# Performance work log

Hardware: AMD Instinct MI355X
Metric: run time of the kernel (lower is better)

## Reference

```python
import jax, jax.numpy as jnp
import numpy as np

N = 100000


def gcn_conv(x, edge_index, W, b):
    """PyG GCNConv: add self-loops, symmetric normalization, x @ W, aggregate, + bias."""
    n = x.shape[0]
    src = jnp.concatenate([edge_index[0], jnp.arange(n)])
    dst = jnp.concatenate([edge_index[1], jnp.arange(n)])
    deg = jax.ops.segment_sum(jnp.ones_like(dst, dtype=x.dtype), dst, num_segments=n)
    dinv = jnp.where(deg > 0, jax.lax.rsqrt(deg), 0.0)
    norm = dinv[src] * dinv[dst]  # [E+N]
    h = x @ W  # [N, out]
    msg = h[src] * norm[:, None]  # gather + scale
    agg = jax.ops.segment_sum(msg, dst, num_segments=n)
    return agg + b


def setup_inputs() -> dict:
    key = jax.random.key(0)
    ks = jax.random.split(key, 10)
    x = jax.random.normal(ks[0], (N, 256), dtype=jnp.float32)
    edge_index = jax.random.randint(ks[1], (2, 3200000), 0, N, dtype=jnp.int64)
    def glorot(k, fan_in, fan_out):
        s = np.sqrt(6.0 / (fan_in + fan_out)).astype(np.float32)
        return jax.random.uniform(k, (fan_in, fan_out), jnp.float32, -s, s)
    return {
        "x": x,
        "edge_index": edge_index,
        "W1": glorot(ks[2], 256, 128), "b1": jnp.zeros((128,), jnp.float32),
        "W2": glorot(ks[3], 128, 64), "b2": jnp.zeros((64,), jnp.float32),
        "W3": glorot(ks[4], 64, 16), "b3": jnp.zeros((16,), jnp.float32),
        "Wc": glorot(ks[5], 16, 2), "bc": jnp.zeros((2,), jnp.float32),
    }


def reference(x, edge_index, W1, b1, W2, b2, W3, b3, Wc, bc):
    h = jnp.tanh(gcn_conv(x, edge_index, W1, b1))
    h = jnp.tanh(gcn_conv(h, edge_index, W2, b2))
    h = jnp.tanh(gcn_conv(h, edge_index, W3, b3))
    out = h @ Wc + bc
    return (out, h)
```

## Files before the change

### kernel.cpp

```cpp
#include <hip/hip_runtime.h>
#include <hip/hip_fp16.h>
#include <cstdint>
#include <cstddef>


#define EPB 16384
#define BSHIFT 8
#define NBUC_MAX 512
#define BCAP 12800

typedef __attribute__((ext_vector_type(8))) short short8;
typedef __attribute__((ext_vector_type(4))) float f32x4;

__global__ __launch_bounds__(256) void scan_block(const int* __restrict__ src, int n,
                                                  int* __restrict__ incl,
                                                  int* __restrict__ bsum) {
    int tid = threadIdx.x;
    int v = blockIdx.x * 256 + tid;
    int val = (v < n) ? src[v] : 0;
    int lane = tid & 63, w = tid >> 6;
#pragma unroll
    for (int off = 1; off < 64; off <<= 1) {
        int t = __shfl_up(val, off, 64);
        if (lane >= off) val += t;
    }
    __shared__ int wsum[4];
    if (lane == 63) wsum[w] = val;
    __syncthreads();
#pragma unroll
    for (int i = 0; i < 4; ++i)
        if (i < w) val += wsum[i];
    if (v < n) incl[v] = val;
    if (tid == 255) bsum[blockIdx.x] = val;
}

__global__ __launch_bounds__(512) void scan_sums(int* __restrict__ bsum, int nb) {
    int tid = threadIdx.x;
    int val = (tid < nb) ? bsum[tid] : 0;
    int lane = tid & 63, w = tid >> 6;
#pragma unroll
    for (int off = 1; off < 64; off <<= 1) {
        int t = __shfl_up(val, off, 64);
        if (lane >= off) val += t;
    }
    __shared__ int wsum[8];
    if (lane == 63) wsum[w] = val;
    __syncthreads();
#pragma unroll
    for (int i = 0; i < 8; ++i)
        if (i < w) val += wsum[i];
    if (tid < nb) bsum[tid] = val;
}

__global__ __launch_bounds__(256) void finalize_scan(
    const int* __restrict__ incl, const int* __restrict__ bsum,
    const int* __restrict__ src, int n, int* __restrict__ excl) {
    int v = blockIdx.x * 256 + threadIdx.x;
    if (v >= n) return;
    int boff = (blockIdx.x == 0) ? 0 : bsum[blockIdx.x - 1];
    excl[v] = boff + incl[v] - src[v];
}

__global__ __launch_bounds__(256) void hist_bucket(
    const int* __restrict__ ei, int E, int nbuc, int nch,
    int* __restrict__ histG) {
    __shared__ int h[NBUC_MAX];
    const int k = blockIdx.x;
    for (int b = threadIdx.x; b < NBUC_MAX; b += 256) h[b] = 0;
    __syncthreads();
    const int base = k * EPB, end = min(E, base + EPB);
    for (int i = base + threadIdx.x; i < end; i += 256)
        atomicAdd(&h[ei[(size_t)E + i] >> BSHIFT], 1);
    __syncthreads();
    for (int b = threadIdx.x; b < nbuc; b += 256)
        histG[(size_t)b * nch + k] = h[b];
}

__global__ __launch_bounds__(256) void bucket_scatter(
    const int* __restrict__ ei, int E, int nbuc, int nch,
    const int* __restrict__ offs, uint2* __restrict__ ebuf) {
    __shared__ int cur[NBUC_MAX];
    const int k = blockIdx.x;
    for (int b = threadIdx.x; b < nbuc; b += 256)
        cur[b] = offs[(size_t)b * nch + k];
    __syncthreads();
    const int base = k * EPB, end = min(E, base + EPB);
    for (int i = base + threadIdx.x; i < end; i += 256) {
        int s = ei[i];
        int d = ei[(size_t)E + i];
        int pos = atomicAdd(&cur[d >> BSHIFT], 1);
        ebuf[pos] = make_uint2((unsigned)s, (unsigned)d);
    }
}

__global__ __launch_bounds__(256) void bucket_build(
    const uint2* __restrict__ ebuf, const int* __restrict__ offs,
    int E, int nbuc, int nch, int n,
    int* __restrict__ col, int* __restrict__ deg,
    int* __restrict__ row_start, float* __restrict__ dinv) {
    const int b = blockIdx.x;
    const int tid = threadIdx.x;
    const int estart = offs[(size_t)b * nch];
    const int eend = (b + 1 < nbuc) ? offs[(size_t)(b + 1) * nch] : E;
    const int cnt = eend - estart;

    __shared__ int degl[256];
    __shared__ int curl[256];
    __shared__ int wsum[4];
    __shared__ int colstage[BCAP];

    degl[tid] = 0;
    __syncthreads();
    for (int i = tid; i < cnt; i += 256)
        atomicAdd(&degl[ebuf[estart + i].y & 255], 1);
    __syncthreads();
    int myDeg = degl[tid];
    int val = myDeg;
    int lane = tid & 63, w = tid >> 6;
#pragma unroll
    for (int off = 1; off < 64; off <<= 1) {
        int t = __shfl_up(val, off, 64);
        if (lane >= off) val += t;
    }
    if (lane == 63) wsum[w] = val;
    __syncthreads();
#pragma unroll
    for (int i = 0; i < 4; ++i)
        if (i < w) val += wsum[i];
    int excl = val - myDeg;
    curl[tid] = excl;
    int v = (b << BSHIFT) + tid;
    if (v < n) {
        deg[v] = myDeg;
        row_start[v] = estart + excl;
        dinv[v] = rsqrtf((float)(myDeg + 1));
    }
    __syncthreads();
    if (cnt <= BCAP) {
        for (int i = tid; i < cnt; i += 256) {
            uint2 e = ebuf[estart + i];
            int pos = atomicAdd(&curl[e.y & 255], 1);
            colstage[pos] = (int)e.x;
        }
        __syncthreads();
        for (int i = tid; i < cnt; i += 256)
            col[estart + i] = colstage[i];
    } else {
        for (int i = tid; i < cnt; i += 256) {
            uint2 e = ebuf[estart + i];
            int pos = atomicAdd(&curl[e.y & 255], 1);
            col[estart + pos] = (int)e.x;
        }
    }
}

__device__ inline unsigned int pack2h(float a, float b) {
    __half ha = __float2half_rn(a), hb = __float2half_rn(b);
    unsigned short ua = *(unsigned short*)&ha, ub = *(unsigned short*)&hb;
    return (unsigned int)ua | ((unsigned int)ub << 16);
}

__device__ inline unsigned short f32_to_bf16_rn(float f) {
    unsigned int u = __float_as_uint(f);
    unsigned int r = (u + 0x7FFFu + ((u >> 16) & 1u)) >> 16;
    return (unsigned short)r;
}
__device__ inline float bf16_to_f32(unsigned short h) {
    return __uint_as_float(((unsigned int)h) << 16);
}

template <int FIN, int FOUT>
__global__ __launch_bounds__(256) void pack_w(const float* __restrict__ W,
                                              unsigned short* __restrict__ Wpk) {
    constexpr int KC = FIN / 32, CF = FOUT / 16;
    constexpr int TOT = KC * CF * 64 * 8;
    int idx = blockIdx.x * 256 + threadIdx.x;
    if (idx >= TOT) return;
    int j = idx & 7;
    int lane = (idx >> 3) & 63;
    int cf = (idx >> 9) % CF;
    int kc = (idx >> 9) / CF;
    int k = kc * 32 + ((lane >> 4) * 8) + j;
    int c = cf * 16 + (lane & 15);
    float w = W[(size_t)k * FOUT + c];
    unsigned short h = f32_to_bf16_rn(w);
    unsigned short l = f32_to_bf16_rn(w - bf16_to_f32(h));
    size_t base = ((size_t)((kc * CF + cf) * 64 + lane)) * 16;
    Wpk[base + j] = h;
    Wpk[base + 8 + j] = l;
}

template <int FIN, int FOUT>
__global__ __launch_bounds__(256) void gemm_mfma(
    const float* __restrict__ X, const unsigned short* __restrict__ Wpk,
    const float* __restrict__ dinv, __half* __restrict__ Hs, int n) {
    constexpr int KC = FIN / 32, CF = FOUT / 16, RF = 2;
    constexpr int BM = 4 * RF * 16;
    const int w = threadIdx.x >> 6, lane = threadIdx.x & 63;
    const int g = lane >> 4, rr = lane & 15;
    const int node0 = blockIdx.x * BM + w * (RF * 16);
    const int ko = g * 8;

    f32x4 acc[RF][CF];
#pragma unroll
    for (int rf = 0; rf < RF; ++rf)
#pragma unroll
        for (int cf = 0; cf < CF; ++cf)
            acc[rf][cf] = (f32x4){0.f, 0.f, 0.f, 0.f};

    union U16 { uint4 u; short8 s; };

    for (int kc = 0; kc < KC; ++kc) {
        short8 ahi[RF], alo[RF];
#pragma unroll
        for (int rf = 0; rf < RF; ++rf) {
            int r = node0 + rf * 16 + rr;
            float xv[8] = {0.f, 0.f, 0.f, 0.f, 0.f, 0.f, 0.f, 0.f};
            if (r < n) {
                const float* xp = X + (size_t)r * FIN + kc * 32 + ko;
                float4 a0 = *(const float4*)xp;
                float4 a1 = *(const float4*)(xp + 4);
                xv[0] = a0.x; xv[1] = a0.y; xv[2] = a0.z; xv[3] = a0.w;
                xv[4] = a1.x; xv[5] = a1.y; xv[6] = a1.z; xv[7] = a1.w;
            }
#pragma unroll
            for (int j = 0; j < 8; ++j) {
                unsigned short hb = f32_to_bf16_rn(xv[j]);
                float rem = xv[j] - bf16_to_f32(hb);
                ahi[rf][j] = (short)hb;
                alo[rf][j] = (short)f32_to_bf16_rn(rem);
            }
        }
#pragma unroll
        for (int cf = 0; cf < CF; ++cf) {
            const uint4* bp = (const uint4*)(Wpk +
                ((size_t)((kc * CF + cf) * 64 + lane)) * 16);
            U16 bh, bl;
            bh.u = bp[0];
            bl.u = bp[1];
#pragma unroll
            for (int rf = 0; rf < RF; ++rf) {
                acc[rf][cf] = __builtin_amdgcn_mfma_f32_16x16x32_bf16(
                    ahi[rf], bh.s, acc[rf][cf], 0, 0, 0);
                acc[rf][cf] = __builtin_amdgcn_mfma_f32_16x16x32_bf16(
                    alo[rf], bh.s, acc[rf][cf], 0, 0, 0);
                acc[rf][cf] = __builtin_amdgcn_mfma_f32_16x16x32_bf16(
                    ahi[rf], bl.s, acc[rf][cf], 0, 0, 0);
            }
        }
    }

#pragma unroll
    for (int rf = 0; rf < RF; ++rf) {
#pragma unroll
        for (int i = 0; i < 4; ++i) {
            int r = node0 + rf * 16 + g * 4 + i;
            if (r >= n) continue;
            float di = dinv[r];
            __half* hp = Hs + (size_t)r * FOUT + rr;
#pragma unroll
            for (int cf = 0; cf < CF; ++cf)
                hp[cf * 16] = __float2half_rn(acc[rf][cf][i] * di);
        }
    }
}

template <int FIN, int FOUT, int TM>
__global__ __launch_bounds__(256) void gemm_tile_h(
    const float* __restrict__ X, const float* __restrict__ W,
    const float* __restrict__ dinv, __half* __restrict__ Hs, int n) {
    constexpr int CT = FOUT / 4;
    constexpr int RG = 256 / CT;
    static_assert(TM == RG * 4, "tile mismatch");
    constexpr int LROW = FIN + 4;
    __shared__ float xs[TM][LROW];

    const int node0 = blockIdx.x * TM;
    const int tid = threadIdx.x;

    constexpr int C4 = FIN / 4;
    for (int i = tid; i < TM * C4; i += 256) {
        int r = i / C4, c = i % C4;
        float4 v = make_float4(0.f, 0.f, 0.f, 0.f);
        if (node0 + r < n) v = *(const float4*)(X + (size_t)(node0 + r) * FIN + c * 4);
        *(float4*)&xs[r][c * 4] = v;
    }
    __syncthreads();

    const int col = (tid % CT) * 4;
    const int r0 = (tid / CT) * 4;

    float acc[4][4];
#pragma unroll
    for (int i = 0; i < 4; ++i)
#pragma unroll
        for (int j = 0; j < 4; ++j) acc[i][j] = 0.f;

#pragma unroll 2
    for (int k = 0; k < FIN; k += 4) {
        float4 w0 = *(const float4*)(W + (size_t)(k + 0) * FOUT + col);
        float4 w1 = *(const float4*)(W + (size_t)(k + 1) * FOUT + col);
        float4 w2 = *(const float4*)(W + (size_t)(k + 2) * FOUT + col);
        float4 w3 = *(const float4*)(W + (size_t)(k + 3) * FOUT + col);
        float4 av[4];
        av[0] = *(const float4*)&xs[r0 + 0][k];
        av[1] = *(const float4*)&xs[r0 + 1][k];
        av[2] = *(const float4*)&xs[r0 + 2][k];
        av[3] = *(const float4*)&xs[r0 + 3][k];
#pragma unroll
        for (int rr = 0; rr < 4; ++rr) {
            acc[rr][0] = fmaf(av[rr].x, w0.x, acc[rr][0]);
            acc[rr][1] = fmaf(av[rr].x, w0.y, acc[rr][1]);
            acc[rr][2] = fmaf(av[rr].x, w0.z, acc[rr][2]);
            acc[rr][3] = fmaf(av[rr].x, w0.w, acc[rr][3]);
            acc[rr][0] = fmaf(av[rr].y, w1.x, acc[rr][0]);
            acc[rr][1] = fmaf(av[rr].y, w1.y, acc[rr][1]);
            acc[rr][2] = fmaf(av[rr].y, w1.z, acc[rr][2]);
            acc[rr][3] = fmaf(av[rr].y, w1.w, acc[rr][3]);
            acc[rr][0] = fmaf(av[rr].z, w2.x, acc[rr][0]);
            acc[rr][1] = fmaf(av[rr].z, w2.y, acc[rr][1]);
            acc[rr][2] = fmaf(av[rr].z, w2.z, acc[rr][2]);
            acc[rr][3] = fmaf(av[rr].z, w2.w, acc[rr][3]);
            acc[rr][0] = fmaf(av[rr].w, w3.x, acc[rr][0]);
            acc[rr][1] = fmaf(av[rr].w, w3.y, acc[rr][1]);
            acc[rr][2] = fmaf(av[rr].w, w3.z, acc[rr][2]);
            acc[rr][3] = fmaf(av[rr].w, w3.w, acc[rr][3]);
        }
    }

#pragma unroll
    for (int rr = 0; rr < 4; ++rr) {
        int node = node0 + r0 + rr;
        if (node < n) {
            float di = dinv[node];
            uint2 pk;
            pk.x = pack2h(acc[rr][0] * di, acc[rr][1] * di);
            pk.y = pack2h(acc[rr][2] * di, acc[rr][3] * di);
            *(uint2*)(Hs + (size_t)node * FOUT + col) = pk;
        }
    }
}

__device__ inline void add8h(float* acc, uint4 p) {
    unsigned int w[4] = {p.x, p.y, p.z, p.w};
#pragma unroll
    for (int t = 0; t < 4; ++t) {
        __half2 h = *(const __half2*)&w[t];
        float2 f = __half22float2(h);
        acc[2 * t] += f.x;
        acc[2 * t + 1] += f.y;
    }
}

template <int F>
__global__ __launch_bounds__(256) void pull_agg_h(
    const int* __restrict__ row_start, const int* __restrict__ deg,
    const int* __restrict__ col, const __half* __restrict__ Hs,
    const float* __restrict__ dinv, const float* __restrict__ B,
    float* __restrict__ OUT, int n) {
    constexpr int TPE = F / 8;
    long long gid = (long long)blockIdx.x * 256 + threadIdx.x;
    int node = (int)(gid / TPE);
    int lane = (int)(gid % TPE);
    if (node >= n) return;
    const int beg = row_start[node];
    const int cnt = deg[node];
    const size_t lo = (size_t)lane * 8;

    float acc[8] = {0.f, 0.f, 0.f, 0.f, 0.f, 0.f, 0.f, 0.f};
    add8h(acc, *(const uint4*)(Hs + (size_t)node * F + lo));

    int j = 0;
    for (; j + 8 <= cnt; j += 8) {
        int s0 = col[beg + j + 0], s1 = col[beg + j + 1];
        int s2 = col[beg + j + 2], s3 = col[beg + j + 3];
        int s4 = col[beg + j + 4], s5 = col[beg + j + 5];
        int s6 = col[beg + j + 6], s7 = col[beg + j + 7];
        uint4 p0 = *(const uint4*)(Hs + (size_t)s0 * F + lo);
        uint4 p1 = *(const uint4*)(Hs + (size_t)s1 * F + lo);
        uint4 p2 = *(const uint4*)(Hs + (size_t)s2 * F + lo);
        uint4 p3 = *(const uint4*)(Hs + (size_t)s3 * F + lo);
        uint4 p4 = *(const uint4*)(Hs + (size_t)s4 * F + lo);
        uint4 p5 = *(const uint4*)(Hs + (size_t)s5 * F + lo);
        uint4 p6 = *(const uint4*)(Hs + (size_t)s6 * F + lo);
        uint4 p7 = *(const uint4*)(Hs + (size_t)s7 * F + lo);
        add8h(acc, p0); add8h(acc, p1); add8h(acc, p2); add8h(acc, p3);
        add8h(acc, p4); add8h(acc, p5); add8h(acc, p6); add8h(acc, p7);
    }
    for (; j < cnt; ++j) {
        int s = col[beg + j];
        add8h(acc, *(const uint4*)(Hs + (size_t)s * F + lo));
    }

    float di = dinv[node];
    float4 b0 = *(const float4*)(B + lo);
    float4 b1 = *(const float4*)(B + lo + 4);
    float4 r0, r1;
    r0.x = tanhf(fmaf(acc[0], di, b0.x));
    r0.y = tanhf(fmaf(acc[1], di, b0.y));
    r0.z = tanhf(fmaf(acc[2], di, b0.z));
    r0.w = tanhf(fmaf(acc[3], di, b0.w));
    r1.x = tanhf(fmaf(acc[4], di, b1.x));
    r1.y = tanhf(fmaf(acc[5], di, b1.y));
    r1.z = tanhf(fmaf(acc[6], di, b1.z));
    r1.w = tanhf(fmaf(acc[7], di, b1.w));
    float* op = OUT + (size_t)node * F + lo;
    *(float4*)(op) = r0;
    *(float4*)(op + 4) = r1;
}

__global__ void classifier_kernel(const float* __restrict__ Hf,
                                  const float* __restrict__ Wc,
                                  const float* __restrict__ bc,
                                  float* __restrict__ out, int n) {
    int v = blockIdx.x * blockDim.x + threadIdx.x;
    if (v >= n) return;
    float o0 = bc[0], o1 = bc[1];
    const float* h = Hf + (size_t)v * 16;
#pragma unroll
    for (int k = 0; k < 16; ++k) {
        float hv = h[k];
        o0 = fmaf(hv, Wc[k * 2 + 0], o0);
        o1 = fmaf(hv, Wc[k * 2 + 1], o1);
    }
    out[(size_t)v * 2 + 0] = o0;
    out[(size_t)v * 2 + 1] = o1;
}

extern "C" void kernel_launch(void* const* d_in, const int* in_sizes, int n_in,
                              void* d_out, int out_size, void* d_ws, size_t ws_size,
                              hipStream_t stream) {
    const float* x  = (const float*)d_in[0];
    const int* ei   = (const int*)d_in[1];
    const float* W1 = (const float*)d_in[2];
    const float* b1 = (const float*)d_in[3];
    const float* W2 = (const float*)d_in[4];
    const float* b2 = (const float*)d_in[5];
    const float* W3 = (const float*)d_in[6];
    const float* b3 = (const float*)d_in[7];
    const float* Wc = (const float*)d_in[8];
    const float* bc = (const float*)d_in[9];

    const int n = in_sizes[0] / 256;
    const int E = in_sizes[1] / 2;
    const int nbuc = (n + 255) >> BSHIFT;
    const int nch  = (E + EPB - 1) / EPB;
    const int NH   = nbuc * nch;
    const int nb2  = (NH + 255) / 256;

    float* outp = (float*)d_out;
    float* outh = outp + (size_t)n * 2;

    int*    deg       = (int*)d_ws;
    float*  dinv      = (float*)d_ws + (size_t)n;
    int*    row_start = (int*)d_ws + 2 * (size_t)n;
    int*    histG     = (int*)d_ws + 3 * (size_t)n;
    int*    incl      = histG + NH;
    int*    bsum      = incl + NH;
    int*    offs      = bsum + 512;
    int*    col       = offs + NH;
    __half* HsH       = (__half*)(col + E);
    float*  xbuf      = (float*)(HsH + (size_t)n * 128);
    uint2*  ebuf      = (uint2*)xbuf;

    unsigned short* Wpk1 = (unsigned short*)histG;
    unsigned short* Wpk2 = Wpk1 + (size_t)256 * 128 * 2;

    hist_bucket<<<nch, 256, 0, stream>>>(ei, E, nbuc, nch, histG);
    scan_block<<<nb2, 256, 0, stream>>>(histG, NH, incl, bsum);
    scan_sums<<<1, 512, 0, stream>>>(bsum, nb2);
    finalize_scan<<<nb2, 256, 0, stream>>>(incl, bsum, histG, NH, offs);
    bucket_scatter<<<nch, 256, 0, stream>>>(ei, E, nbuc, nch, offs, ebuf);
    bucket_build<<<nbuc, 256, 0, stream>>>(ebuf, offs, E, nbuc, nch, n,
                                           col, deg, row_start, dinv);

    pack_w<256, 128><<<(256 / 32 * 128 / 16 * 512 + 255) / 256, 256, 0, stream>>>(W1, Wpk1);
    pack_w<128, 64><<<(128 / 32 * 64 / 16 * 512 + 255) / 256, 256, 0, stream>>>(W2, Wpk2);

    gemm_mfma<256, 128><<<(n + 127) / 128, 256, 0, stream>>>(x, Wpk1, dinv, HsH, n);
    pull_agg_h<128><<<(int)(((long long)n * 16 + 255) / 256), 256, 0, stream>>>(
        row_start, deg, col, HsH, dinv, b1, xbuf, n);

    gemm_mfma<128, 64><<<(n + 127) / 128, 256, 0, stream>>>(xbuf, Wpk2, dinv, HsH, n);
    pull_agg_h<64><<<(int)(((long long)n * 8 + 255) / 256), 256, 0, stream>>>(
        row_start, deg, col, HsH, dinv, b2, xbuf, n);

    gemm_tile_h<64, 16, 256><<<(n + 255) / 256, 256, 0, stream>>>(xbuf, W3, dinv, HsH, n);
    pull_agg_h<16><<<(int)(((long long)n * 2 + 255) / 256), 256, 0, stream>>>(
        row_start, deg, col, HsH, dinv, b3, outh, n);

    classifier_kernel<<<(n + 255) / 256, 256, 0, stream>>>(outh, Wc, bc, outp, n);
}
```

Baseline: 637.6 us.

## Split hidden features into 16-wide planes and aggregate plane by plane

```diff
diff --git a/kernel.cpp b/kernel.cpp
--- a/kernel.cpp
+++ b/kernel.cpp
@@ -78,7 +78,7 @@
 
 __global__ __launch_bounds__(256) void bucket_scatter(
     const int* __restrict__ ei, int E, int nbuc, int nch,
-    const int* __restrict__ offs, uint2* __restrict__ ebuf) {
+    const int* __restrict__ offs, unsigned int* __restrict__ ebuf) {
     __shared__ int cur[NBUC_MAX];
     const int k = blockIdx.x;
     for (int b = threadIdx.x; b < nbuc; b += 256)
@@ -89,12 +89,12 @@
         int s = ei[i];
         int d = ei[(size_t)E + i];
         int pos = atomicAdd(&cur[d >> BSHIFT], 1);
-        ebuf[pos] = make_uint2((unsigned)s, (unsigned)d);
+        ebuf[pos] = (unsigned)s | ((unsigned)(d & 255) << 24);
     }
 }
 
 __global__ __launch_bounds__(256) void bucket_build(
-    const uint2* __restrict__ ebuf, const int* __restrict__ offs,
+    const unsigned int* __restrict__ ebuf, const int* __restrict__ offs,
     int E, int nbuc, int nch, int n,
     int* __restrict__ col, int* __restrict__ deg,
     int* __restrict__ row_start, float* __restrict__ dinv) {
@@ -112,7 +112,7 @@
     degl[tid] = 0;
     __syncthreads();
     for (int i = tid; i < cnt; i += 256)
-        atomicAdd(&degl[ebuf[estart + i].y & 255], 1);
+        atomicAdd(&degl[ebuf[estart + i] >> 24], 1);
     __syncthreads();
     int myDeg = degl[tid];
     int val = myDeg;
@@ -138,26 +138,20 @@
     __syncthreads();
     if (cnt <= BCAP) {
         for (int i = tid; i < cnt; i += 256) {
-            uint2 e = ebuf[estart + i];
-            int pos = atomicAdd(&curl[e.y & 255], 1);
-            colstage[pos] = (int)e.x;
+            unsigned int e = ebuf[estart + i];
+            int pos = atomicAdd(&curl[e >> 24], 1);
+            colstage[pos] = (int)(e & 0xFFFFFFu);
         }
         __syncthreads();
         for (int i = tid; i < cnt; i += 256)
             col[estart + i] = colstage[i];
     } else {
         for (int i = tid; i < cnt; i += 256) {
-            uint2 e = ebuf[estart + i];
-            int pos = atomicAdd(&curl[e.y & 255], 1);
-            col[estart + pos] = (int)e.x;
-        }
-    }
-}
-
-__device__ inline unsigned int pack2h(float a, float b) {
-    __half ha = __float2half_rn(a), hb = __float2half_rn(b);
-    unsigned short ua = *(unsigned short*)&ha, ub = *(unsigned short*)&hb;
-    return (unsigned int)ua | ((unsigned int)ub << 16);
+            unsigned int e = ebuf[estart + i];
+            int pos = atomicAdd(&curl[e >> 24], 1);
+            col[estart + pos] = (int)(e & 0xFFFFFFu);
+        }
+    }
 }
 
 __device__ inline unsigned short f32_to_bf16_rn(float f) {
@@ -190,7 +184,7 @@
     Wpk[base + 8 + j] = l;
 }
 
-template <int FIN, int FOUT>
+template <int FIN, int FOUT, bool PBIN>
 __global__ __launch_bounds__(256) void gemm_mfma(
     const float* __restrict__ X, const unsigned short* __restrict__ Wpk,
     const float* __restrict__ dinv, __half* __restrict__ Hs, int n) {
@@ -217,7 +211,13 @@
             int r = node0 + rf * 16 + rr;
             float xv[8] = {0.f, 0.f, 0.f, 0.f, 0.f, 0.f, 0.f, 0.f};
             if (r < n) {
-                const float* xp = X + (size_t)r * FIN + kc * 32 + ko;
+                const float* xp;
+                if (!PBIN) {
+                    xp = X + (size_t)r * FIN + kc * 32 + ko;
+                } else {
+                    int plane = 2 * kc + (g >> 1);
+                    xp = X + ((size_t)plane * n + r) * 16 + (g & 1) * 8;
+                }
                 float4 a0 = *(const float4*)xp;
                 float4 a1 = *(const float4*)(xp + 4);
                 xv[0] = a0.x; xv[1] = a0.y; xv[2] = a0.z; xv[3] = a0.w;
@@ -225,10 +225,10 @@
             }
 #pragma unroll
             for (int j = 0; j < 8; ++j) {
-                unsigned short hb = f32_to_bf16_rn(xv[j]);
-                float rem = xv[j] - bf16_to_f32(hb);
-                ahi[rf][j] = (short)hb;
-                alo[rf][j] = (short)f32_to_bf16_rn(rem);
+                unsigned int u = __float_as_uint(xv[j]);
+                ahi[rf][j] = (short)(unsigned short)(u >> 16);
+                float hf = __uint_as_float(u & 0xFFFF0000u);
+                alo[rf][j] = (short)f32_to_bf16_rn(xv[j] - hf);
             }
         }
 #pragma unroll
@@ -257,15 +257,15 @@
             int r = node0 + rf * 16 + g * 4 + i;
             if (r >= n) continue;
             float di = dinv[r];
-            __half* hp = Hs + (size_t)r * FOUT + rr;
 #pragma unroll
             for (int cf = 0; cf < CF; ++cf)
-                hp[cf * 16] = __float2half_rn(acc[rf][cf][i] * di);
-        }
-    }
-}
-
-template <int FIN, int FOUT, int TM>
+                Hs[((size_t)cf * n + r) * 16 + rr] =
+                    __float2half_rn(acc[rf][cf][i] * di);
+        }
+    }
+}
+
+template <int FIN, int FOUT, int TM, bool PBIN>
 __global__ __launch_bounds__(256) void gemm_tile_h(
     const float* __restrict__ X, const float* __restrict__ W,
     const float* __restrict__ dinv, __half* __restrict__ Hs, int n) {
@@ -280,10 +280,16 @@
 
     constexpr int C4 = FIN / 4;
     for (int i = tid; i < TM * C4; i += 256) {
-        int r = i / C4, c = i % C4;
+        int r = i / C4, c4 = i % C4;
+        int c = c4 * 4;
         float4 v = make_float4(0.f, 0.f, 0.f, 0.f);
-        if (node0 + r < n) v = *(const float4*)(X + (size_t)(node0 + r) * FIN + c * 4);
-        *(float4*)&xs[r][c * 4] = v;
+        if (node0 + r < n) {
+            const float* xp;
+            if (!PBIN) xp = X + (size_t)(node0 + r) * FIN + c;
+            else       xp = X + ((size_t)(c >> 4) * n + node0 + r) * 16 + (c & 15);
+            v = *(const float4*)xp;
+        }
+        *(float4*)&xs[r][c] = v;
     }
     __syncthreads();
 
@@ -333,9 +339,15 @@
         int node = node0 + r0 + rr;
         if (node < n) {
             float di = dinv[node];
+            __half h0 = __float2half_rn(acc[rr][0] * di);
+            __half h1 = __float2half_rn(acc[rr][1] * di);
+            __half h2 = __float2half_rn(acc[rr][2] * di);
+            __half h3 = __float2half_rn(acc[rr][3] * di);
+            unsigned short u0 = *(unsigned short*)&h0, u1 = *(unsigned short*)&h1;
+            unsigned short u2 = *(unsigned short*)&h2, u3 = *(unsigned short*)&h3;
             uint2 pk;
-            pk.x = pack2h(acc[rr][0] * di, acc[rr][1] * di);
-            pk.y = pack2h(acc[rr][2] * di, acc[rr][3] * di);
+            pk.x = (unsigned)u0 | ((unsigned)u1 << 16);
+            pk.y = (unsigned)u2 | ((unsigned)u3 << 16);
             *(uint2*)(Hs + (size_t)node * FOUT + col) = pk;
         }
     }
@@ -352,23 +364,20 @@
     }
 }
 
-template <int F>
-__global__ __launch_bounds__(256) void pull_agg_h(
+__global__ __launch_bounds__(256) void pull_plane(
     const int* __restrict__ row_start, const int* __restrict__ deg,
-    const int* __restrict__ col, const __half* __restrict__ Hs,
-    const float* __restrict__ dinv, const float* __restrict__ B,
-    float* __restrict__ OUT, int n) {
-    constexpr int TPE = F / 8;
-    long long gid = (long long)blockIdx.x * 256 + threadIdx.x;
-    int node = (int)(gid / TPE);
-    int lane = (int)(gid % TPE);
+    const int* __restrict__ col, const __half* __restrict__ Hp,
+    const float* __restrict__ dinv, const float* __restrict__ Bp,
+    float* __restrict__ OUTp, int n) {
+    int gid = blockIdx.x * 256 + threadIdx.x;
+    int node = gid >> 1;
     if (node >= n) return;
+    const size_t lo = (size_t)(gid & 1) * 8;
     const int beg = row_start[node];
     const int cnt = deg[node];
-    const size_t lo = (size_t)lane * 8;
 
     float acc[8] = {0.f, 0.f, 0.f, 0.f, 0.f, 0.f, 0.f, 0.f};
-    add8h(acc, *(const uint4*)(Hs + (size_t)node * F + lo));
+    add8h(acc, *(const uint4*)(Hp + (size_t)node * 16 + lo));
 
     int j = 0;
     for (; j + 8 <= cnt; j += 8) {
@@ -376,25 +385,25 @@
         int s2 = col[beg + j + 2], s3 = col[beg + j + 3];
         int s4 = col[beg + j + 4], s5 = col[beg + j + 5];
         int s6 = col[beg + j + 6], s7 = col[beg + j + 7];
-        uint4 p0 = *(const uint4*)(Hs + (size_t)s0 * F + lo);
-        uint4 p1 = *(const uint4*)(Hs + (size_t)s1 * F + lo);
-        uint4 p2 = *(const uint4*)(Hs + (size_t)s2 * F + lo);
-        uint4 p3 = *(const uint4*)(Hs + (size_t)s3 * F + lo);
-        uint4 p4 = *(const uint4*)(Hs + (size_t)s4 * F + lo);
-        uint4 p5 = *(const uint4*)(Hs + (size_t)s5 * F + lo);
-        uint4 p6 = *(const uint4*)(Hs + (size_t)s6 * F + lo);
-        uint4 p7 = *(const uint4*)(Hs + (size_t)s7 * F + lo);
+        uint4 p0 = *(const uint4*)(Hp + (size_t)s0 * 16 + lo);
+        uint4 p1 = *(const uint4*)(Hp + (size_t)s1 * 16 + lo);
+        uint4 p2 = *(const uint4*)(Hp + (size_t)s2 * 16 + lo);
+        uint4 p3 = *(const uint4*)(Hp + (size_t)s3 * 16 + lo);
+        uint4 p4 = *(const uint4*)(Hp + (size_t)s4 * 16 + lo);
+        uint4 p5 = *(const uint4*)(Hp + (size_t)s5 * 16 + lo);
+        uint4 p6 = *(const uint4*)(Hp + (size_t)s6 * 16 + lo);
+        uint4 p7 = *(const uint4*)(Hp + (size_t)s7 * 16 + lo);
         add8h(acc, p0); add8h(acc, p1); add8h(acc, p2); add8h(acc, p3);
         add8h(acc, p4); add8h(acc, p5); add8h(acc, p6); add8h(acc, p7);
     }
     for (; j < cnt; ++j) {
         int s = col[beg + j];
-        add8h(acc, *(const uint4*)(Hs + (size_t)s * F + lo));
+        add8h(acc, *(const uint4*)(Hp + (size_t)s * 16 + lo));
     }
 
     float di = dinv[node];
-    float4 b0 = *(const float4*)(B + lo);
-    float4 b1 = *(const float4*)(B + lo + 4);
+    float4 b0 = *(const float4*)(Bp + lo);
+    float4 b1 = *(const float4*)(Bp + lo + 4);
     float4 r0, r1;
     r0.x = tanhf(fmaf(acc[0], di, b0.x));
     r0.y = tanhf(fmaf(acc[1], di, b0.y));
@@ -404,27 +413,72 @@
     r1.y = tanhf(fmaf(acc[5], di, b1.y));
     r1.z = tanhf(fmaf(acc[6], di, b1.z));
     r1.w = tanhf(fmaf(acc[7], di, b1.w));
-    float* op = OUT + (size_t)node * F + lo;
+    float* op = OUTp + (size_t)node * 16 + lo;
     *(float4*)(op) = r0;
     *(float4*)(op + 4) = r1;
 }
 
-__global__ void classifier_kernel(const float* __restrict__ Hf,
-                                  const float* __restrict__ Wc,
-                                  const float* __restrict__ bc,
-                                  float* __restrict__ out, int n) {
-    int v = blockIdx.x * blockDim.x + threadIdx.x;
-    if (v >= n) return;
-    float o0 = bc[0], o1 = bc[1];
-    const float* h = Hf + (size_t)v * 16;
-#pragma unroll
-    for (int k = 0; k < 16; ++k) {
-        float hv = h[k];
-        o0 = fmaf(hv, Wc[k * 2 + 0], o0);
-        o1 = fmaf(hv, Wc[k * 2 + 1], o1);
-    }
-    out[(size_t)v * 2 + 0] = o0;
-    out[(size_t)v * 2 + 1] = o1;
+__global__ __launch_bounds__(256) void pull_cls(
+    const int* __restrict__ row_start, const int* __restrict__ deg,
+    const int* __restrict__ col, const __half* __restrict__ Hs,
+    const float* __restrict__ dinv, const float* __restrict__ B,
+    const float* __restrict__ Wc, const float* __restrict__ bc,
+    float* __restrict__ OUTH, float* __restrict__ OUTC, int n) {
+    int gid = blockIdx.x * 256 + threadIdx.x;
+    int node = gid >> 1;
+    if (node >= n) return;
+    const int half = gid & 1;
+    const size_t lo = (size_t)half * 8;
+    const int beg = row_start[node];
+    const int cnt = deg[node];
+
+    float acc[8] = {0.f, 0.f, 0.f, 0.f, 0.f, 0.f, 0.f, 0.f};
+    add8h(acc, *(const uint4*)(Hs + (size_t)node * 16 + lo));
+
+    int j = 0;
+    for (; j + 8 <= cnt; j += 8) {
+        int s0 = col[beg + j + 0], s1 = col[beg + j + 1];
+        int s2 = col[beg + j + 2], s3 = col[beg + j + 3];
+        int s4 = col[beg + j + 4], s5 = col[beg + j + 5];
+        int s6 = col[beg + j + 6], s7 = col[beg + j + 7];
+        uint4 p0 = *(const uint4*)(Hs + (size_t)s0 * 16 + lo);
+        uint4 p1 = *(const uint4*)(Hs + (size_t)s1 * 16 + lo);
+        uint4 p2 = *(const uint4*)(Hs + (size_t)s2 * 16 + lo);
+        uint4 p3 = *(const uint4*)(Hs + (size_t)s3 * 16 + lo);
+        uint4 p4 = *(const uint4*)(Hs + (size_t)s4 * 16 + lo);
+        uint4 p5 = *(const uint4*)(Hs + (size_t)s5 * 16 + lo);
+        uint4 p6 = *(const uint4*)(Hs + (size_t)s6 * 16 + lo);
+        uint4 p7 = *(const uint4*)(Hs + (size_t)s7 * 16 + lo);
+        add8h(acc, p0); add8h(acc, p1); add8h(acc, p2); add8h(acc, p3);
+        add8h(acc, p4); add8h(acc, p5); add8h(acc, p6); add8h(acc, p7);
+    }
+    for (; j < cnt; ++j) {
+        int s = col[beg + j];
+        add8h(acc, *(const uint4*)(Hs + (size_t)s * 16 + lo));
+    }
+
+    float di = dinv[node];
+    float r[8];
+#pragma unroll
+    for (int k = 0; k < 8; ++k)
+        r[k] = tanhf(fmaf(acc[k], di, B[lo + k]));
+
+    float* op = OUTH + (size_t)node * 16 + lo;
+    *(float4*)(op)     = make_float4(r[0], r[1], r[2], r[3]);
+    *(float4*)(op + 4) = make_float4(r[4], r[5], r[6], r[7]);
+
+    float o0 = 0.f, o1 = 0.f;
+#pragma unroll
+    for (int k = 0; k < 8; ++k) {
+        o0 = fmaf(r[k], Wc[(lo + k) * 2 + 0], o0);
+        o1 = fmaf(r[k], Wc[(lo + k) * 2 + 1], o1);
+    }
+    o0 += __shfl_xor(o0, 1);
+    o1 += __shfl_xor(o1, 1);
+    if (half == 0) {
+        OUTC[(size_t)node * 2 + 0] = o0 + bc[0];
+        OUTC[(size_t)node * 2 + 1] = o1 + bc[1];
+    }
 }
 
 extern "C" void kernel_launch(void* const* d_in, const int* in_sizes, int n_in,
@@ -461,7 +515,7 @@
     int*    col       = offs + NH;
     __half* HsH       = (__half*)(col + E);
     float*  xbuf      = (float*)(HsH + (size_t)n * 128);
-    uint2*  ebuf      = (uint2*)xbuf;
+    unsigned int* ebuf = (unsigned int*)xbuf;
 
     unsigned short* Wpk1 = (unsigned short*)histG;
     unsigned short* Wpk2 = Wpk1 + (size_t)256 * 128 * 2;
@@ -477,17 +531,21 @@
     pack_w<256, 128><<<(256 / 32 * 128 / 16 * 512 + 255) / 256, 256, 0, stream>>>(W1, Wpk1);
     pack_w<128, 64><<<(128 / 32 * 64 / 16 * 512 + 255) / 256, 256, 0, stream>>>(W2, Wpk2);
 
-    gemm_mfma<256, 128><<<(n + 127) / 128, 256, 0, stream>>>(x, Wpk1, dinv, HsH, n);
-    pull_agg_h<128><<<(int)(((long long)n * 16 + 255) / 256), 256, 0, stream>>>(
-        row_start, deg, col, HsH, dinv, b1, xbuf, n);
-
-    gemm_mfma<128, 64><<<(n + 127) / 128, 256, 0, stream>>>(xbuf, Wpk2, dinv, HsH, n);
-    pull_agg_h<64><<<(int)(((long long)n * 8 + 255) / 256), 256, 0, stream>>>(
-        row_start, deg, col, HsH, dinv, b2, xbuf, n);
-
-    gemm_tile_h<64, 16, 256><<<(n + 255) / 256, 256, 0, stream>>>(xbuf, W3, dinv, HsH, n);
-    pull_agg_h<16><<<(int)(((long long)n * 2 + 255) / 256), 256, 0, stream>>>(
-        row_start, deg, col, HsH, dinv, b3, outh, n);
-
-    classifier_kernel<<<(n + 255) / 256, 256, 0, stream>>>(outh, Wc, bc, outp, n);
-}
+    const int pgrid = (2 * n + 255) / 256;
+
+    gemm_mfma<256, 128, false><<<(n + 127) / 128, 256, 0, stream>>>(x, Wpk1, dinv, HsH, n);
+    for (int p = 0; p < 8; ++p)
+        pull_plane<<<pgrid, 256, 0, stream>>>(
+            row_start, deg, col, HsH + (size_t)p * n * 16, dinv,
+            b1 + p * 16, xbuf + (size_t)p * n * 16, n);
+
+    gemm_mfma<128, 64, true><<<(n + 127) / 128, 256, 0, stream>>>(xbuf, Wpk2, dinv, HsH, n);
+    for (int p = 0; p < 4; ++p)
+        pull_plane<<<pgrid, 256, 0, stream>>>(
+            row_start, deg, col, HsH + (size_t)p * n * 16, dinv,
+            b2 + p * 16, xbuf + (size_t)p * n * 16, n);
+
+    gemm_tile_h<64, 16, 256, true><<<(n + 255) / 256, 256, 0, stream>>>(xbuf, W3, dinv, HsH, n);
+    pull_cls<<<pgrid, 256, 0, stream>>>(row_start, deg, col, HsH, dinv, b3,
+                                        Wc, bc, outh, outp, n);
+}
```

Result: slower. 803.1 us (+25.9%).
